# Kernel optimization log

Measured on AMD Instinct MI355X. Metric: run time of the kernel, lower is better.

## Reference

```python
import jax, jax.numpy as jnp
import numpy as np


def setup_inputs() -> dict:
    key = jax.random.key(0)
    k1, k2 = jax.random.split(key)
    # [batch, seq, in_features] activations
    x = jax.random.normal(k1, (4, 4096, 2048), dtype=jnp.float32)
    # fp32 master weight [out_features, in_features]; quantized inside reference
    weight = jax.random.normal(k2, (2048, 2048), dtype=jnp.float32) * 0.02
    return {"x": x, "weight": weight}


def reference(x, weight):
    num_bits = 8
    Qn = -(2 ** (num_bits - 1))       # -128
    Qp = 2 ** (num_bits - 1) - 1      # 127

    # Per-row absmax int8 activation quantization (activation_quant)
    si = Qp / jnp.clip(jnp.max(jnp.abs(x), axis=-1, keepdims=True), 1e-5)  # [B,S,1]
    qx = jnp.clip(jnp.round(x * si), Qn, Qp)  # int8 values held in fp32 (exact)

    # Ternary weight quantization (weight_quant): sw scalar = 1/mean|W|
    sw = 1.0 / jnp.clip(jnp.mean(jnp.abs(weight)), 1e-5)
    qw = jnp.clip(jnp.round(weight * sw), -1.0, 1.0)  # {-1,0,1}

    acc = jnp.einsum("bsk,nk->bsn", qx, qw)  # [B,S,out]

    # post_quant_process: dequantize by si and sw, cast to half
    out = ((acc / si) / sw).astype(jnp.float16)
    return out
```

## Files before the change

kernel.cpp:

```cpp
#include <hip/hip_runtime.h>

#define K_DIM 2048
#define N_DIM 2048
#define M_DIM 16384

typedef int v4i __attribute__((ext_vector_type(4)));
typedef int v16i __attribute__((ext_vector_type(16)));


__device__ __forceinline__ void lds16(const void* g, void* l) {
    __builtin_amdgcn_global_load_lds(
        (const __attribute__((address_space(1))) unsigned int*)g,
        (__attribute__((address_space(3))) unsigned int*)l,
        16, 0, 0);
}

__global__ __launch_bounds__(256) void k_wsum(const float* __restrict__ w,
                                              double* __restrict__ part) {
    int tid = blockIdx.x * 256 + threadIdx.x;
    const float4* w4 = (const float4*)w;
    double s = 0.0;
    for (int i = tid; i < (N_DIM * K_DIM / 4); i += 65536) {
        float4 v = w4[i];
        s += (double)fabsf(v.x);
        s += (double)fabsf(v.y);
        s += (double)fabsf(v.z);
        s += (double)fabsf(v.w);
    }
#pragma unroll
    for (int off = 32; off; off >>= 1) s += __shfl_xor(s, off, 64);
    __shared__ double sp[4];
    int lane = threadIdx.x & 63, wv = threadIdx.x >> 6;
    if (lane == 0) sp[wv] = s;
    __syncthreads();
    if (threadIdx.x == 0) part[blockIdx.x] = sp[0] + sp[1] + sp[2] + sp[3];
}

__global__ __launch_bounds__(256) void k_quant_w(const float* __restrict__ w,
                                                 signed char* __restrict__ qw_t,
                                                 const double* __restrict__ part,
                                                 float* __restrict__ invsw_out) {
    double s = part[threadIdx.x];
#pragma unroll
    for (int off = 32; off; off >>= 1) s += __shfl_xor(s, off, 64);
    __shared__ double sp[4];
    __shared__ float s_invsw;
    int lane = threadIdx.x & 63, wv = threadIdx.x >> 6;
    if (lane == 0) sp[wv] = s;
    __syncthreads();
    if (threadIdx.x == 0) {
        double total = sp[0] + sp[1] + sp[2] + sp[3];
        float mean = (float)(total * (1.0 / (double)(N_DIM * K_DIM)));
        s_invsw = fmaxf(mean, 1e-5f);
        if (blockIdx.x == 0) *invsw_out = s_invsw;
    }
    __syncthreads();
    float sw = 1.0f / s_invsw;

    int row = blockIdx.x * 4 + wv;
    const float4* wr_ = (const float4*)(w + (size_t)row * K_DIM);
    int bn = row >> 7, ri = row & 127;
    signed char* base = qw_t + (size_t)bn * 262144 + (((lane >> 2) & 3) << 11) + (ri << 4) + ((lane & 3) << 2);
    int ksBase = lane >> 4;
#pragma unroll
    for (int c = 0; c < 8; c++) {
        float4 v = wr_[c * 64 + lane];
        int q0 = (int)fminf(fmaxf(rintf(v.x * sw), -1.f), 1.f);
        int q1 = (int)fminf(fmaxf(rintf(v.y * sw), -1.f), 1.f);
        int q2 = (int)fminf(fmaxf(rintf(v.z * sw), -1.f), 1.f);
        int q3 = (int)fminf(fmaxf(rintf(v.w * sw), -1.f), 1.f);
        int q = (q0 & 255) | ((q1 & 255) << 8) | ((q2 & 255) << 16) | ((q3 & 255) << 24);
        *(int*)(base + (size_t)(4 * c + ksBase) * 8192) = q;
    }
}

__global__ __launch_bounds__(256) void k_quant_x(const float* __restrict__ x,
                                                 signed char* __restrict__ qx_t,
                                                 float* __restrict__ si_out) {
    int row = blockIdx.x * 4 + (threadIdx.x >> 6);
    int lane = threadIdx.x & 63;
    const float4* xr = (const float4*)(x + (size_t)row * K_DIM);
    float4 v[8];
    float mx = 0.f;
#pragma unroll
    for (int c = 0; c < 8; c++) {
        v[c] = xr[c * 64 + lane];
        mx = fmaxf(mx, fmaxf(fmaxf(fabsf(v[c].x), fabsf(v[c].y)),
                             fmaxf(fabsf(v[c].z), fabsf(v[c].w))));
    }
#pragma unroll
    for (int off = 32; off; off >>= 1) mx = fmaxf(mx, __shfl_xor(mx, off, 64));
    float si = 127.0f / fmaxf(mx, 1e-5f);
    if (lane == 0) si_out[row] = si;

    int bm = row >> 8, ri = row & 255;
    signed char* base = qx_t + (size_t)bm * 524288 + (((lane >> 2) & 3) << 12) + (ri << 4) + ((lane & 3) << 2);
    int ksBase = lane >> 4;
#pragma unroll
    for (int c = 0; c < 8; c++) {
        int q0 = (int)fminf(fmaxf(rintf(v[c].x * si), -128.f), 127.f);
        int q1 = (int)fminf(fmaxf(rintf(v[c].y * si), -128.f), 127.f);
        int q2 = (int)fminf(fmaxf(rintf(v[c].z * si), -128.f), 127.f);
        int q3 = (int)fminf(fmaxf(rintf(v[c].w * si), -128.f), 127.f);
        int q = (q0 & 255) | ((q1 & 255) << 8) | ((q2 & 255) << 16) | ((q3 & 255) << 24);
        *(int*)(base + (size_t)(4 * c + ksBase) * 16384) = q;
    }
}

__global__ __launch_bounds__(256, 2) void k_gemm(const signed char* __restrict__ qx_t,
                                                 const signed char* __restrict__ qw_t,
                                                 const float* __restrict__ si,
                                                 const float* __restrict__ invsw_p,
                                                 float* __restrict__ out) {
    __shared__ __align__(16) signed char As[2][16384];
    __shared__ __align__(16) signed char Bs[2][8192];
    const int t = threadIdx.x;
    const int lane = t & 63, wv = t >> 6;
    const int wr = wv >> 1, wc = wv & 1;
    const int l31 = lane & 31, lh = lane >> 5;
    const int bn = blockIdx.x, bm = blockIdx.y;

    const signed char* aT = qx_t + (size_t)bm * 524288;
    const signed char* bT = qw_t + (size_t)bn * 262144;
    const int t16 = t << 4;

#define STAGE(buf, ksv)                                      \
    {                                                        \
        const signed char* aS = aT + ((size_t)(ksv) << 14);  \
        const signed char* bS = bT + ((size_t)(ksv) << 13);  \
        signed char* Ad = As[buf];                           \
        signed char* Bd = Bs[buf];                           \
        lds16(aS + t16,         Ad + t16);                   \
        lds16(aS + 4096 + t16,  Ad + 4096 + t16);            \
        lds16(aS + 8192 + t16,  Ad + 8192 + t16);            \
        lds16(aS + 12288 + t16, Ad + 12288 + t16);           \
        lds16(bS + t16,         Bd + t16);                   \
        lds16(bS + 4096 + t16,  Bd + 4096 + t16);            \
    }

    v16i acc[4][2] = {};

    STAGE(0, 0);
    __syncthreads();

    for (int ks = 0; ks < 32; ks++) {
        const int cur = ks & 1;
        if (ks < 31) STAGE(cur ^ 1, ks + 1);

        const signed char* Ac = As[cur];
        const signed char* Bc = Bs[cur];
#pragma unroll
        for (int ks2 = 0; ks2 < 2; ks2++) {
            v4i af[4], bf[2];
#pragma unroll
            for (int mt = 0; mt < 4; mt++)
                af[mt] = *(const v4i*)(Ac + (((ks2 * 2 + lh) * 256 + wr * 128 + mt * 32 + l31) << 4));
#pragma unroll
            for (int nt = 0; nt < 2; nt++)
                bf[nt] = *(const v4i*)(Bc + (((ks2 * 2 + lh) * 128 + wc * 64 + nt * 32 + l31) << 4));
#pragma unroll
            for (int mt = 0; mt < 4; mt++)
#pragma unroll
                for (int nt = 0; nt < 2; nt++)
                    acc[mt][nt] = __builtin_amdgcn_mfma_i32_32x32x32_i8(af[mt], bf[nt], acc[mt][nt], 0, 0, 0);
        }
        __syncthreads();
    }
#undef STAGE

    float invsw = *invsw_p;
#pragma unroll
    for (int mt = 0; mt < 4; mt++) {
        int rowb = bm * 256 + wr * 128 + mt * 32 + (lh << 2);
        float sc[16];
#pragma unroll
        for (int r = 0; r < 16; r++)
            sc[r] = invsw / si[rowb + (r & 3) + ((r >> 2) << 3)];
#pragma unroll
        for (int nt = 0; nt < 2; nt++) {
            int col = bn * 128 + wc * 64 + nt * 32 + l31;
#pragma unroll
            for (int r = 0; r < 16; r++) {
                int row = rowb + (r & 3) + ((r >> 2) << 3);
                float vv = (float)acc[mt][nt][r] * sc[r];
                out[(size_t)row * N_DIM + col] = (float)(_Float16)vv;
            }
        }
    }
}

extern "C" void kernel_launch(void* const* d_in, const int* in_sizes, int n_in,
                              void* d_out, int out_size, void* d_ws, size_t ws_size,
                              hipStream_t stream) {
    const float* x = (const float*)d_in[0];
    const float* w = (const float*)d_in[1];
    float* out = (float*)d_out;
    char* ws = (char*)d_ws;

    double* part = (double*)ws;
    float* invsw = (float*)(ws + 2048);
    float* si = (float*)(ws + 4096);
    signed char* qw_t = (signed char*)(ws + 4096 + 65536);
    signed char* qx_t = qw_t + (size_t)N_DIM * K_DIM;

    k_wsum<<<256, 256, 0, stream>>>(w, part);
    k_quant_x<<<4096, 256, 0, stream>>>(x, qx_t, si);
    k_quant_w<<<512, 256, 0, stream>>>(w, qw_t, part, invsw);
    k_gemm<<<dim3(N_DIM / 128, M_DIM / 256), 256, 0, stream>>>(qx_t, qw_t, si, invsw, out);
}
```

Before: 346.3 us.

## Triple-buffer A tiles with explicit vmcnt waits and swizzle block order

The GEMM main loop now keeps three LDS buffers for the activation tile and two for the weight tile. A prefetches two k-steps ahead and B one step ahead. Fixed s_waitcnt vmcnt counts and raw s_barrier calls replace __syncthreads, so some global-to-LDS loads can stay in flight while MFMAs run. The grid is flattened to 1D and remapped so that consecutive workgroups share weight tiles and land on different XCD groups, which should improve L2 reuse. The costs are more LDS per block, which may cut occupancy from 2 blocks per CU, and correctness that depends on the hand-counted vmcnt values.

```diff
diff --git a/kernel.cpp b/kernel.cpp
--- a/kernel.cpp
+++ b/kernel.cpp
@@ -112,61 +112,97 @@
                                                  const float* __restrict__ si,
                                                  const float* __restrict__ invsw_p,
                                                  float* __restrict__ out) {
-    __shared__ __align__(16) signed char As[2][16384];
+    __shared__ __align__(16) signed char As[3][16384];
     __shared__ __align__(16) signed char Bs[2][8192];
     const int t = threadIdx.x;
     const int lane = t & 63, wv = t >> 6;
     const int wr = wv >> 1, wc = wv & 1;
     const int l31 = lane & 31, lh = lane >> 5;
-    const int bn = blockIdx.x, bm = blockIdx.y;
+
+    const int wg = blockIdx.x;
+    const int swz = (wg & 7) * 128 + (wg >> 3);
+    const int bn = swz & 15, bm = swz >> 4;
 
     const signed char* aT = qx_t + (size_t)bm * 524288;
     const signed char* bT = qw_t + (size_t)bn * 262144;
     const int t16 = t << 4;
 
-#define STAGE(buf, ksv)                                      \
+#define STAGE_A(buf, ksv)                                    \
     {                                                        \
         const signed char* aS = aT + ((size_t)(ksv) << 14);  \
-        const signed char* bS = bT + ((size_t)(ksv) << 13);  \
         signed char* Ad = As[buf];                           \
-        signed char* Bd = Bs[buf];                           \
         lds16(aS + t16,         Ad + t16);                   \
         lds16(aS + 4096 + t16,  Ad + 4096 + t16);            \
         lds16(aS + 8192 + t16,  Ad + 8192 + t16);            \
         lds16(aS + 12288 + t16, Ad + 12288 + t16);           \
+    }
+#define STAGE_B(buf, ksv)                                    \
+    {                                                        \
+        const signed char* bS = bT + ((size_t)(ksv) << 13);  \
+        signed char* Bd = Bs[buf];                           \
         lds16(bS + t16,         Bd + t16);                   \
         lds16(bS + 4096 + t16,  Bd + 4096 + t16);            \
     }
 
     v16i acc[4][2] = {};
 
-    STAGE(0, 0);
-    __syncthreads();
-
-    for (int ks = 0; ks < 32; ks++) {
-        const int cur = ks & 1;
-        if (ks < 31) STAGE(cur ^ 1, ks + 1);
-
-        const signed char* Ac = As[cur];
-        const signed char* Bc = Bs[cur];
-#pragma unroll
-        for (int ks2 = 0; ks2 < 2; ks2++) {
-            v4i af[4], bf[2];
-#pragma unroll
-            for (int mt = 0; mt < 4; mt++)
-                af[mt] = *(const v4i*)(Ac + (((ks2 * 2 + lh) * 256 + wr * 128 + mt * 32 + l31) << 4));
-#pragma unroll
-            for (int nt = 0; nt < 2; nt++)
-                bf[nt] = *(const v4i*)(Bc + (((ks2 * 2 + lh) * 128 + wc * 64 + nt * 32 + l31) << 4));
-#pragma unroll
-            for (int mt = 0; mt < 4; mt++)
-#pragma unroll
-                for (int nt = 0; nt < 2; nt++)
-                    acc[mt][nt] = __builtin_amdgcn_mfma_i32_32x32x32_i8(af[mt], bf[nt], acc[mt][nt], 0, 0, 0);
-        }
-        __syncthreads();
-    }
-#undef STAGE
+#define COMPUTE(AC, BC)                                                                              \
+    {                                                                                                \
+        const signed char* Ac = As[AC];                                                              \
+        const signed char* Bc = Bs[BC];                                                              \
+        _Pragma("unroll")                                                                            \
+        for (int ks2 = 0; ks2 < 2; ks2++) {                                                          \
+            v4i af[4], bf[2];                                                                        \
+            _Pragma("unroll")                                                                        \
+            for (int mt = 0; mt < 4; mt++)                                                           \
+                af[mt] = *(const v4i*)(Ac + (((ks2 * 2 + lh) * 256 + wr * 128 + mt * 32 + l31) << 4)); \
+            _Pragma("unroll")                                                                        \
+            for (int nt = 0; nt < 2; nt++)                                                           \
+                bf[nt] = *(const v4i*)(Bc + (((ks2 * 2 + lh) * 128 + wc * 64 + nt * 32 + l31) << 4)); \
+            _Pragma("unroll")                                                                        \
+            for (int mt = 0; mt < 4; mt++)                                                           \
+                _Pragma("unroll")                                                                    \
+                for (int nt = 0; nt < 2; nt++)                                                       \
+                    acc[mt][nt] = __builtin_amdgcn_mfma_i32_32x32x32_i8(af[mt], bf[nt], acc[mt][nt], 0, 0, 0); \
+        }                                                                                            \
+    }
+
+#define ITER10(ksv, AC, BC, AS, BS)                          \
+    {                                                        \
+        STAGE_B(BS, (ksv) + 1);                              \
+        STAGE_A(AS, (ksv) + 2);                              \
+        asm volatile("s_waitcnt vmcnt(10)" ::: "memory");    \
+        __builtin_amdgcn_s_barrier();                        \
+        COMPUTE(AC, BC);                                     \
+        __builtin_amdgcn_s_barrier();                        \
+    }
+
+    STAGE_B(0, 0);
+    STAGE_A(0, 0);
+    STAGE_A(1, 1);
+
+    for (int ks = 0; ks < 30; ks += 6) {
+        ITER10(ks + 0, 0, 0, 2, 1);
+        ITER10(ks + 1, 1, 1, 0, 0);
+        ITER10(ks + 2, 2, 0, 1, 1);
+        ITER10(ks + 3, 0, 1, 2, 0);
+        ITER10(ks + 4, 1, 0, 0, 1);
+        ITER10(ks + 5, 2, 1, 1, 0);
+    }
+
+    STAGE_B(1, 31);
+    asm volatile("s_waitcnt vmcnt(6)" ::: "memory");
+    __builtin_amdgcn_s_barrier();
+    COMPUTE(0, 0);
+    __builtin_amdgcn_s_barrier();
+    asm volatile("s_waitcnt vmcnt(0)" ::: "memory");
+    __builtin_amdgcn_s_barrier();
+    COMPUTE(1, 1);
+
+#undef ITER10
+#undef COMPUTE
+#undef STAGE_A
+#undef STAGE_B
 
     float invsw = *invsw_p;
 #pragma unroll
@@ -206,5 +242,5 @@
     k_wsum<<<256, 256, 0, stream>>>(w, part);
     k_quant_x<<<4096, 256, 0, stream>>>(x, qx_t, si);
     k_quant_w<<<512, 256, 0, stream>>>(w, qw_t, part, invsw);
-    k_gemm<<<dim3(N_DIM / 128, M_DIM / 256), 256, 0, stream>>>(qx_t, qw_t, si, invsw, out);
-}
+    k_gemm<<<1024, 256, 0, stream>>>(qx_t, qw_t, si, invsw, out);
+}
```

New measurement: 323.2 us. 6.7% less time.
